# Performance work log

Measured on AMD Instinct MI355X. Metric: run time of the kernel, lower is better.

The kernel has to match this reference:

```python
import jax, jax.numpy as jnp
import numpy as np

EPS = 1e-5

# The 8 fixed sobel kernels from the original module. Summing convolutions with
# the same input equals one convolution with the summed kernel, so we embed the
# four 3x3 kernels (pad=1) into 5x5 (pad=2) and precombine everything into a
# single depthwise 5x5 kernel (exactly the math of detect_edge_1/2 summed).
_K3 = [
    [[2, 4, 2], [0, 0, 0], [-2, -4, -2]],
    [[4, 2, 0], [2, 0, -2], [0, -2, -4]],
    [[2, 0, -2], [4, 0, -4], [2, 0, -2]],
    [[0, -2, -4], [2, 0, -2], [4, 2, 0]],
]
_K5 = [
    [[0, 0, 0, 0, 0], [0, -2, -4, -2, 0], [-1, -4, 0, 4, 1], [0, 2, 4, 2, 0], [0, 0, 0, 0, 0]],
    [[0, 0, -1, 0, 0], [0, -2, -4, 2, 0], [0, -4, 0, 4, 0], [0, -2, 4, 2, 0], [0, 0, 1, 0, 0]],
    [[0, 0, 1, 0, 0], [0, -2, 4, 2, 0], [0, -4, 0, 4, 0], [0, -2, -4, 2, 0], [0, 0, -1, 0, 0]],
    [[0, 0, 0, 0, 0], [0, 2, 4, 2, 0], [-1, -4, 0, 4, 1], [0, -2, -4, -2, 0], [0, 0, 0, 0, 0]],
]

def _combined_sobel_kernel():
    k = np.zeros((5, 5), dtype=np.float32)
    for k3 in _K3:
        k[1:4, 1:4] += np.asarray(k3, dtype=np.float32)
    for k5 in _K5:
        k += np.asarray(k5, dtype=np.float32)
    return jnp.asarray(k)

SOBEL_K = _combined_sobel_kernel()  # [5,5]


def _conv2d(x, w, b, pad):
    # x: [N,C,H,W], w: [O,I,kh,kw]
    y = jax.lax.conv_general_dilated(
        x, w, window_strides=(1, 1), padding=[(pad, pad), (pad, pad)],
        dimension_numbers=('NCHW', 'OIHW', 'NCHW'))
    return y + b[None, :, None, None]


def _bn_relu(y, gamma, beta):
    # BatchNorm2d in training mode: per-channel batch stats over (N,H,W),
    # biased variance, eps=1e-5.
    m = jnp.mean(y, axis=(0, 2, 3), keepdims=True)
    v = jnp.mean(jnp.square(y - m), axis=(0, 2, 3), keepdims=True)
    yn = (y - m) * jax.lax.rsqrt(v + EPS)
    return jax.nn.relu(yn * gamma[None, :, None, None] + beta[None, :, None, None])


def _single_conv(x, w, b, gamma, beta, pad):
    return _bn_relu(_conv2d(x, w, b, pad), gamma, beta)


def _sobel(x):
    # Fused depthwise conv replacing the per-channel loops over 8 kernels.
    C = x.shape[1]
    w = jnp.broadcast_to(SOBEL_K[None, None], (C, 1, 5, 5))
    return jax.lax.conv_general_dilated(
        x, w, window_strides=(1, 1), padding=[(2, 2), (2, 2)],
        dimension_numbers=('NCHW', 'OIHW', 'NCHW'), feature_group_count=C)


def setup_inputs() -> dict:
    key = jax.random.key(0)
    ks = jax.random.split(key, 16)
    Cin, Cout = 64, 128
    Ch = Cout // 2
    B, H, W = 8, 160, 160
    s = 0.05
    d = {
        'input_f': jax.random.normal(ks[0], (B, Cin, H, W), jnp.float32),
        'w1': jax.random.normal(ks[1], (Cout, Cin, 1, 1), jnp.float32) * s,
        'b1': jnp.zeros((Cout,), jnp.float32),
        'g1': jnp.ones((Cout,), jnp.float32),
        'be1': jnp.zeros((Cout,), jnp.float32),
        'w2': jax.random.normal(ks[2], (Ch, Cout, 3, 3), jnp.float32) * s,
        'b2': jnp.zeros((Ch,), jnp.float32),
        'g2': jnp.ones((Ch,), jnp.float32),
        'be2': jnp.zeros((Ch,), jnp.float32),
        'w3': jax.random.normal(ks[3], (Ch, Ch, 3, 3), jnp.float32) * s,
        'b3': jnp.zeros((Ch,), jnp.float32),
        'g3': jnp.ones((Ch,), jnp.float32),
        'be3': jnp.zeros((Ch,), jnp.float32),
        'w4': jax.random.normal(ks[4], (Ch, Cin, 3, 3), jnp.float32) * s,
        'b4': jnp.zeros((Ch,), jnp.float32),
        'g4': jnp.ones((Ch,), jnp.float32),
        'be4': jnp.zeros((Ch,), jnp.float32),
    }
    return d


def reference(input_f, w1, b1, g1, be1, w2, b2, g2, be2, w3, b3, g3, be3, w4, b4, g4, be4):
    c1 = _single_conv(input_f, w1, b1, g1, be1, pad=0)   # [B,Cout,H,W]
    c2 = _single_conv(c1, w2, b2, g2, be2, pad=1)        # [B,Cout//2,H,W]
    edge = _sobel(c2)                                    # depthwise sobel sum
    c3 = _single_conv(edge, w3, b3, g3, be3, pad=1)
    skip = _single_conv(input_f, w4, b4, g4, be4, pad=1)
    return jnp.concatenate([skip, c3], axis=1)           # [B,Cout,H,W]
```

## Files before the change

### kernel.cpp

```cpp
#include <hip/hip_runtime.h>

typedef unsigned short u16;
typedef unsigned int u32;
typedef __attribute__((ext_vector_type(8))) short bf16x8;
typedef __attribute__((ext_vector_type(4))) float f32x4;

#define WD 160
#define HW 25600
#define NPIXF 204800.0f
#define BNEPS 1e-5f
#define SLOTB 6553600ll
#define BATB  13107200ll

__device__ __forceinline__ float bf2f(u16 u){ return __uint_as_float(((u32)u)<<16); }
__device__ __forceinline__ u16 f2bf(float f){ u32 x=__float_as_uint(f); return (u16)((x + 0x7FFFu + ((x>>16)&1u))>>16); }
__device__ __forceinline__ u32 pack2(float a,float b){ return (u32)f2bf(a) | ((u32)f2bf(b)<<16); }

__device__ __forceinline__ f32x4 MF(bf16x8 a, bf16x8 b, f32x4 c){
  return __builtin_amdgcn_mfma_f32_16x16x32_bf16(a, b, c, 0, 0, 0);
}
__device__ __forceinline__ void gload16(const void* g, void* l){
  __builtin_amdgcn_global_load_lds((const __attribute__((address_space(1))) void*)(g),
                                   (__attribute__((address_space(3))) void*)(l), 16, 0, 0);
}

__global__ __launch_bounds__(256) void k_prepw(
    const float* __restrict__ w1, const float* __restrict__ w2,
    const float* __restrict__ w3, const float* __restrict__ w4,
    u16* __restrict__ wp1, u16* __restrict__ wp2,
    u16* __restrict__ wp3, u16* __restrict__ wp4)
{
  int t = blockIdx.x*256 + threadIdx.x;
  if (t < 8192){
    int i = t&7, oc = (t>>3)&127, kc = (t>>10)&3, icb = t>>12;
    wp1[t] = f2bf(w1[oc*64 + icb*32 + kc*8 + i]);
  }
  int u = t - 8192;
  if (u >= 0 && u < 73728){
    int i = u&7, oc = (u>>3)&63, kc = (u>>9)&3, v = u>>11;
    int icb = (v*57)>>9; int tap = v - icb*9;
    wp2[u] = f2bf(w2[(oc*128 + icb*32 + kc*8 + i)*9 + tap]);
  }
  int u3 = t - (8192+73728);
  if (u3 >= 0 && u3 < 36864){
    int k = u3&31, oc = (u3>>5)&63, v = u3>>11;
    int icb = (v >= 9) ? 1 : 0; int tap = v - icb*9;
    int phys = u3 ^ (((oc>>1)&3)<<3);
    wp3[phys] = f2bf(w3[(oc*64 + icb*32 + k)*9 + tap]);
    wp4[phys] = f2bf(w4[(oc*64 + icb*32 + k)*9 + tap]);
  }
}

__global__ __launch_bounds__(256,2) void k_conv1(
    const float* __restrict__ x, const u16* __restrict__ wp1,
    char* __restrict__ dout, float* __restrict__ stats, int nslot)
{
  __shared__ __align__(16) char Xs[16384];
  __shared__ __align__(16) char Ws[8192];
  const int tid = threadIdx.x, lane = tid&63, w = tid>>6;
  const int l15 = lane&15, kc = lane>>4;
  const int b = blockIdx.y, px0 = blockIdx.x*256;
  const float* xb = x + (size_t)b*64*HW;

  f32x4 acc[4][8];
  for (int t=0;t<4;++t) for (int o=0;o<8;++o) acc[t][o] = (f32x4){0.f,0.f,0.f,0.f};

  int a1off[4];
  for (int t=0;t<4;++t){
    int px = (w*4+t)*16 + l15;
    a1off[t] = px*64 + ((kc ^ ((px>>1)&3))<<4);
  }
  const int wboff = kc*2048 + l15*16;

  for (int icb=0; icb<2; ++icb){
    __syncthreads();
    for (int it=0; it<16; ++it){
      int s = it*256 + tid;
      int icp = s >> 8, px = s & 255;
      const float* p = xb + (size_t)(icb*32 + icp*2)*HW + px0 + px;
      float v0 = p[0], v1 = p[HW];
      int phys = px*64 + (((icp>>2) ^ ((px>>1)&3))<<4) + (icp&3)*4;
      *(u32*)(Xs + phys) = pack2(v0, v1);
    }
    for (int it=0; it<2; ++it){
      int s = it*256 + tid;
      gload16(wp1 + (size_t)icb*4096 + s*8, Ws + (it*256 + (tid & ~63))*16);
    }
    asm volatile("s_waitcnt vmcnt(0)" ::: "memory");
    __syncthreads();
    bf16x8 a[4], bv[8];
#pragma unroll
    for (int t=0;t<4;++t) a[t] = *(const bf16x8*)(Xs + a1off[t]);
#pragma unroll
    for (int o=0;o<8;++o) bv[o] = *(const bf16x8*)(Ws + o*256 + wboff);
#pragma unroll
    for (int t=0;t<4;++t)
#pragma unroll
      for (int o=0;o<8;++o)
        acc[t][o] = MF(a[t], bv[o], acc[t][o]);
  }

  u16* c1 = (u16*)(dout + (size_t)b*BATB);
  float sa[8], sq[8];
  for (int o=0;o<8;++o){ sa[o]=0.f; sq[o]=0.f; }
  for (int t=0;t<4;++t){
    int pxb = px0 + (w*4+t)*16 + kc*4;
    for (int o=0;o<8;++o){
      int oc = o*16 + l15;
#pragma unroll
      for (int r=0;r<4;++r){
        float v = acc[t][o][r];
        c1[(size_t)(pxb + r)*128 + oc] = f2bf(v);
        sa[o]+=v; sq[o]+=v*v;
      }
    }
  }
  const int slot = (blockIdx.y*gridDim.x + blockIdx.x) & (nslot-1);
  for (int o=0;o<8;++o){
    float s1_=sa[o], s2_=sq[o];
    s1_+=__shfl_xor(s1_,16); s2_+=__shfl_xor(s2_,16);
    s1_+=__shfl_xor(s1_,32); s2_+=__shfl_xor(s2_,32);
    if (lane < 16){
      float* p = stats + ((size_t)slot*128 + o*16 + l15)*4;
      atomicAdd(p, s1_); atomicAdd(p+1, s2_);
    }
  }
}

__global__ void k_fold(const float* __restrict__ src, float* __restrict__ dst, int nslot){
  int c = threadIdx.x; if (c >= 128) return;
  float sm=0.f, sq=0.f;
  for (int s=0;s<nslot;++s){ const float* p = src + ((size_t)s*128 + c)*4; sm+=p[0]; sq+=p[1]; }
  dst[c*2] = sm; dst[c*2+1] = sq;
}

__global__ __launch_bounds__(256) void k_bn1(
    char* __restrict__ dout, const float* __restrict__ f1,
    const float* __restrict__ g1, const float* __restrict__ be1)
{
  __shared__ float asc[128], abi[128];
  int tid = threadIdx.x;
  if (tid < 128){
    float m = f1[tid*2]/NPIXF;
    float v = f1[tid*2+1]/NPIXF - m*m;
    float sc = g1[tid]*rsqrtf(v + BNEPS);
    asc[tid] = sc; abi[tid] = be1[tid] - m*sc;
  }
  __syncthreads();
  int b = blockIdx.y;
  size_t r = ((size_t)blockIdx.x*256 + tid)*8;
  int c0 = (int)(r & 127);
  const u16* src = (const u16*)(dout + (size_t)b*BATB) + r;
  u16* dst = (u16*)(dout + (size_t)b*BATB + SLOTB) + r;
  uint4 q = *(const uint4*)src;
  u32 wv[4] = {q.x,q.y,q.z,q.w};
#pragma unroll
  for (int j=0;j<4;++j){
    float lo = bf2f((u16)(wv[j]&0xFFFFu)), hi = bf2f((u16)(wv[j]>>16));
    lo = fmaxf(0.f, lo*asc[c0+2*j]   + abi[c0+2*j]);
    hi = fmaxf(0.f, hi*asc[c0+2*j+1] + abi[c0+2*j+1]);
    wv[j] = pack2(lo, hi);
  }
  *(uint4*)dst = make_uint4(wv[0],wv[1],wv[2],wv[3]);
}

__global__ __launch_bounds__(256,2) void k_conv2(
    char* __restrict__ dout, const u16* __restrict__ wp2,
    float* __restrict__ statsO, const u16* __restrict__ zeros, int nslot)
{
  __shared__ __align__(16) char Xs[24576];
  __shared__ __align__(16) char Ws[36864];
  const int tid = threadIdx.x, lane = tid&63, w = tid>>6;
  const int l15 = lane&15, kc = lane>>4;
  const int b = blockIdx.z, gx0 = blockIdx.x*32, gy0 = blockIdx.y*8;
  const u16* c1a = (const u16*)(dout + (size_t)b*BATB + SLOTB);
  u16* raw2 = (u16*)(dout + (size_t)b*BATB);

  f32x4 acc[4][4];
  for (int t=0;t<4;++t) for (int o=0;o<4;++o) acc[t][o] = (f32x4){0.f,0.f,0.f,0.f};

  int xon[2][3];
  for (int h=0;h<2;++h) for (int dx=0;dx<3;++dx){
    int xi = l15 + h*16 + dx;
    xon[h][dx] = xi*64 + ((kc ^ ((xi>>1)&3))<<4);
  }
  const int wboff = kc*1024 + l15*16;

  for (int icb=0; icb<4; ++icb){
    __syncthreads();
    for (int it=0; it<6; ++it){
      int s = it*256 + tid;
      int p = s>>2, sub = s&3;
      int yy = (int)(((u32)p*241u)>>13);
      int xi = p - yy*34;
      int gy = gy0 - 1 + yy, gx = gx0 - 1 + xi;
      int c = sub ^ ((xi>>1)&3);
      const u16* src = zeros;
      if (p < 340 && (unsigned)gy < 160u && (unsigned)gx < 160u)
        src = c1a + ((size_t)(gy*WD+gx)*128 + icb*32 + c*8);
      gload16(src, Xs + (it*256 + (tid & ~63))*16);
    }
    for (int it=0; it<9; ++it){
      int s = it*256 + tid;
      gload16(wp2 + (size_t)icb*18432 + s*8, Ws + (it*256 + (tid & ~63))*16);
    }
    asm volatile("s_waitcnt vmcnt(0)" ::: "memory");
    __syncthreads();
#pragma unroll
    for (int tap=0; tap<9; ++tap){
      const int dy = tap/3, dx = tap - dy*3;
      bf16x8 a[4], bv[4];
#pragma unroll
      for (int t=0;t<4;++t)
        a[t] = *(const bf16x8*)(Xs + (2*w + (t>>1) + dy)*2176 + xon[t&1][dx]);
#pragma unroll
      for (int o=0;o<4;++o)
        bv[o] = *(const bf16x8*)(Ws + tap*4096 + o*256 + wboff);
#pragma unroll
      for (int t=0;t<4;++t)
#pragma unroll
        for (int o=0;o<4;++o)
          acc[t][o] = MF(a[t], bv[o], acc[t][o]);
    }
  }

  float sa[4]={0,0,0,0}, sq[4]={0,0,0,0};
  for (int t=0;t<4;++t){
    int gy = gy0 + 2*w + (t>>1);
    int gxb = gx0 + (t&1)*16 + kc*4;
    for (int o=0;o<4;++o){
      int oc = o*16 + l15;
#pragma unroll
      for (int r=0;r<4;++r){
        float v = acc[t][o][r];
        raw2[(size_t)(gy*WD + gxb + r)*64 + oc] = f2bf(v);
        sa[o]+=v; sq[o]+=v*v;
      }
    }
  }
  int slot = (blockIdx.x + 5*(blockIdx.y + 20*blockIdx.z)) & (nslot-1);
  for (int o=0;o<4;++o){
    float s1_=sa[o], s2_=sq[o];
    s1_+=__shfl_xor(s1_,16); s2_+=__shfl_xor(s2_,16);
    s1_+=__shfl_xor(s1_,32); s2_+=__shfl_xor(s2_,32);
    if (lane<16){
      float* p = statsO + ((size_t)slot*128 + o*16 + l15)*4;
      atomicAdd(p,s1_); atomicAdd(p+1,s2_);
    }
  }
}

__global__ __launch_bounds__(256) void k_sobel(
    char* __restrict__ dout, const float* __restrict__ f2,
    const float* __restrict__ g2, const float* __restrict__ be2)
{
  __shared__ float asc[64], abi[64];
  int tid = threadIdx.x;
  if (tid < 64){
    float m = f2[tid*2]/NPIXF, v = f2[tid*2+1]/NPIXF - m*m;
    float sc = g2[tid]*rsqrtf(v+BNEPS);
    asc[tid]=sc; abi[tid]=be2[tid]-m*sc;
  }
  __syncthreads();
  int b = blockIdx.z, cb = blockIdx.y;
  int px = blockIdx.x*256 + tid;
  int y = (int)(((u32)px*52429u)>>23);
  int x = px - y*WD;
  const u16* raw2 = (const u16*)(dout + (size_t)b*BATB);
  u16* edge = (u16*)(dout + (size_t)b*BATB + 3276800);
  float av[8] = {0,0,0,0,0,0,0,0};
  auto TAP = [&](int dy, int dx, float wt){
    int yy = y+dy, xx = x+dx;
    if ((unsigned)yy>=160u || (unsigned)xx>=160u) return;
    uint4 q = *(const uint4*)(raw2 + ((size_t)(yy*WD+xx)*64 + cb*8));
    u32 ww[4] = {q.x,q.y,q.z,q.w};
#pragma unroll
    for (int j=0;j<4;++j){
      float lo = bf2f((u16)(ww[j]&0xFFFFu)), hi = bf2f((u16)(ww[j]>>16));
      lo = fmaxf(0.f, lo*asc[cb*8+2*j]   + abi[cb*8+2*j]);
      hi = fmaxf(0.f, hi*asc[cb*8+2*j+1] + abi[cb*8+2*j+1]);
      av[2*j]   += wt*lo;
      av[2*j+1] += wt*hi;
    }
  };
  TAP(-1,-1,4.f); TAP(-1,0,4.f);
  TAP(0,-2,-2.f); TAP(0,-1,-8.f); TAP(0,1,8.f); TAP(0,2,2.f);
  TAP(1,0,-4.f);  TAP(1,1,-4.f);
  uint4 o;
  o.x = pack2(av[0],av[1]); o.y = pack2(av[2],av[3]);
  o.z = pack2(av[4],av[5]); o.w = pack2(av[6],av[7]);
  *(uint4*)(edge + ((size_t)px*64 + cb*8)) = o;
}

template<bool XIN>
__global__ __launch_bounds__(256,2) void k_conv34(
    char* __restrict__ dout, const float* __restrict__ x,
    const u16* __restrict__ wp, float* __restrict__ statsO,
    const u16* __restrict__ zeros, int nslot)
{
  __shared__ __align__(16) char Xs[24576];
  __shared__ __align__(16) char Ws[36864];
  const int tid = threadIdx.x, lane = tid&63, w = tid>>6;
  const int l15 = lane&15, kc = lane>>4;
  const int b = blockIdx.z, gx0 = blockIdx.x*32, gy0 = blockIdx.y*8;
  const float* xb = XIN ? (x + (size_t)b*64*HW) : nullptr;
  const u16* edge = XIN ? nullptr : (const u16*)(dout + (size_t)b*BATB + 3276800);
  float* out = XIN ? (float*)(dout + (size_t)b*BATB)
                   : (float*)(dout + (size_t)b*BATB + SLOTB);

  f32x4 acc[4][4];
  for (int m=0;m<4;++m) for (int t=0;t<4;++t) acc[m][t] = (f32x4){0.f,0.f,0.f,0.f};

  int xon[2][3];
  for (int h=0;h<2;++h) for (int dx=0;dx<3;++dx){
    int xi = l15 + h*16 + dx;
    xon[h][dx] = xi*64 + ((kc ^ ((xi>>1)&3))<<4);
  }
  int wko[4];
  for (int m=0;m<4;++m){
    int oc = m*16 + l15;
    wko[m] = oc*64 + ((kc ^ ((oc>>1)&3))<<4);
  }

  for (int icb=0; icb<2; ++icb){
    __syncthreads();
    if (XIN){
      for (int it=0; it<22; ++it){
        int s = it*256 + tid; if (s >= 5440) break;
        int yq = (int)(((u32)(s>>5)*965u)>>14);
        int rem = s - yq*544;
        int icp = (int)(((u32)rem*241u)>>13);
        int xi = rem - icp*34;
        int gy = gy0-1+yq, gx = gx0-1+xi;
        float v0=0.f, v1=0.f;
        if ((unsigned)gy<160u && (unsigned)gx<160u){
          const float* p = xb + (size_t)(icb*32 + icp*2)*HW + gy*WD + gx;
          v0 = p[0]; v1 = p[HW];
        }
        int phys = (yq*34 + xi)*64 + (((icp>>2) ^ ((xi>>1)&3))<<4) + (icp&3)*4;
        *(u32*)(Xs + phys) = pack2(v0, v1);
      }
    } else {
      for (int it=0; it<6; ++it){
        int s = it*256 + tid;
        int p = s>>2, sub = s&3;
        int yy = (int)(((u32)p*241u)>>13);
        int xi = p - yy*34;
        int gy = gy0-1+yy, gx = gx0-1+xi;
        int c = sub ^ ((xi>>1)&3);
        const u16* src = zeros;
        if (p<340 && (unsigned)gy<160u && (unsigned)gx<160u)
          src = edge + ((size_t)(gy*WD+gx)*64 + icb*32 + c*8);
        gload16(src, Xs + (it*256 + (tid & ~63))*16);
      }
    }
    for (int it=0; it<9; ++it){
      int s = it*256 + tid;
      gload16(wp + (size_t)icb*18432 + s*8, Ws + (it*256 + (tid & ~63))*16);
    }
    asm volatile("s_waitcnt vmcnt(0)" ::: "memory");
    __syncthreads();
#pragma unroll
    for (int tap=0; tap<9; ++tap){
      const int dy = tap/3, dx = tap - dy*3;
      bf16x8 a[4], bv[4];
#pragma unroll
      for (int m=0;m<4;++m) a[m] = *(const bf16x8*)(Ws + tap*4096 + wko[m]);
#pragma unroll
      for (int t=0;t<4;++t) bv[t] = *(const bf16x8*)(Xs + (2*w + (t>>1) + dy)*2176 + xon[t&1][dx]);
#pragma unroll
      for (int m=0;m<4;++m)
#pragma unroll
        for (int t=0;t<4;++t)
          acc[m][t] = MF(a[m], bv[t], acc[m][t]);
    }
  }

  float sa[4][4], sq[4][4];
  for (int m=0;m<4;++m) for (int r=0;r<4;++r){ sa[m][r]=0.f; sq[m][r]=0.f; }
  for (int m=0;m<4;++m){
    for (int t=0;t<4;++t){
      int gy = gy0 + 2*w + (t>>1);
      int gx = gx0 + (t&1)*16 + l15;
#pragma unroll
      for (int r=0;r<4;++r){
        float v = acc[m][t][r];
        out[(size_t)(m*16 + kc*4 + r)*HW + gy*WD + gx] = v;
        sa[m][r]+=v; sq[m][r]+=v*v;
      }
    }
  }
  int slot = (blockIdx.x + 5*(blockIdx.y + 20*blockIdx.z)) & (nslot-1);
  for (int m=0;m<4;++m)
    for (int r=0;r<4;++r){
      float s1_=sa[m][r], s2_=sq[m][r];
      s1_+=__shfl_xor(s1_,1); s2_+=__shfl_xor(s2_,1);
      s1_+=__shfl_xor(s1_,2); s2_+=__shfl_xor(s2_,2);
      s1_+=__shfl_xor(s1_,4); s2_+=__shfl_xor(s2_,4);
      s1_+=__shfl_xor(s1_,8); s2_+=__shfl_xor(s2_,8);
      if (l15==0){
        float* p = statsO + ((size_t)slot*128 + m*16 + kc*4 + r)*4;
        atomicAdd(p,s1_); atomicAdd(p+1,s2_);
      }
    }
}

__global__ __launch_bounds__(256) void k_bnrelu(
    float* __restrict__ io, const float* __restrict__ f3, const float* __restrict__ f4,
    const float* __restrict__ g3, const float* __restrict__ be3,
    const float* __restrict__ g4, const float* __restrict__ be4)
{
  size_t e = ((size_t)blockIdx.x*256 + threadIdx.x)*8;
  int cg = (int)((e/HW) & 127);
  float* p = io + (size_t)blockIdx.y*3276800 + e;
  float sm,sq,gg,bb;
  if (cg>=64){ int c=cg-64; sm=f3[c*2]; sq=f3[c*2+1]; gg=g3[c]; bb=be3[c]; }
  else       {             sm=f4[cg*2]; sq=f4[cg*2+1]; gg=g4[cg]; bb=be4[cg]; }
  float m = sm/NPIXF;
  float v = sq/NPIXF - m*m;
  float sc = gg*rsqrtf(v + BNEPS);
  float bi = bb - m*sc;
  float4 a = *(float4*)p;
  float4 bq = *(float4*)(p+4);
  a.x=fmaxf(0.f,a.x*sc+bi); a.y=fmaxf(0.f,a.y*sc+bi);
  a.z=fmaxf(0.f,a.z*sc+bi); a.w=fmaxf(0.f,a.w*sc+bi);
  bq.x=fmaxf(0.f,bq.x*sc+bi); bq.y=fmaxf(0.f,bq.y*sc+bi);
  bq.z=fmaxf(0.f,bq.z*sc+bi); bq.w=fmaxf(0.f,bq.w*sc+bi);
  *(float4*)p = a;
  *(float4*)(p+4) = bq;
}

extern "C" void kernel_launch(void* const* d_in, const int* in_sizes, int n_in,
                              void* d_out, int out_size, void* d_ws, size_t ws_size,
                              hipStream_t stream)
{
  const float* x   = (const float*)d_in[0];
  const float* w1  = (const float*)d_in[1];
  const float* g1  = (const float*)d_in[3];
  const float* be1 = (const float*)d_in[4];
  const float* w2  = (const float*)d_in[5];
  const float* g2  = (const float*)d_in[7];
  const float* be2 = (const float*)d_in[8];
  const float* w3  = (const float*)d_in[9];
  const float* g3  = (const float*)d_in[11];
  const float* be3 = (const float*)d_in[12];
  const float* w4  = (const float*)d_in[13];
  const float* g4  = (const float*)d_in[15];
  const float* be4 = (const float*)d_in[16];
  (void)in_sizes; (void)n_in; (void)out_size;

  int nslot = 32;
  auto need = [&](int ns)->size_t{
    return (size_t)4*ns*128*4*4 + 4096 + (size_t)(8192+73728+36864+36864)*2 + 256;
  };
  while (nslot > 1 && need(nslot) > ws_size) nslot >>= 1;
  if (need(nslot) > ws_size) return;

  char* ws = (char*)d_ws;
  float* S = (float*)ws;
  size_t stg = (size_t)nslot*128*4;
  float* S0=S, *S1=S+stg, *S2=S+2*stg, *S3=S+3*stg;
  float* F = S + 4*stg;
  u16* wp1 = (u16*)(F + 1024);
  u16* wp2 = wp1 + 8192;
  u16* wp3 = wp2 + 73728;
  u16* wp4 = wp3 + 36864;
  u16* zeros = wp4 + 36864;

  hipMemsetAsync(S, 0, 4*stg*sizeof(float), stream);
  hipMemsetAsync(zeros, 0, 256, stream);

  k_prepw<<<464, 256, 0, stream>>>(w1, w2, w3, w4, wp1, wp2, wp3, wp4);
  k_conv1<<<dim3(100,8), 256, 0, stream>>>(x, wp1, (char*)d_out, S0, nslot);
  k_fold<<<1, 128, 0, stream>>>(S0, F, nslot);
  k_bn1<<<dim3(1600,8), 256, 0, stream>>>((char*)d_out, F, g1, be1);
  k_conv2<<<dim3(5,20,8), 256, 0, stream>>>((char*)d_out, wp2, S1, zeros, nslot);
  k_fold<<<1, 128, 0, stream>>>(S1, F+256, nslot);
  k_sobel<<<dim3(100,8,8), 256, 0, stream>>>((char*)d_out, F+256, g2, be2);
  k_conv34<false><<<dim3(5,20,8), 256, 0, stream>>>((char*)d_out, nullptr, wp3, S2, zeros, nslot);
  k_conv34<true ><<<dim3(5,20,8), 256, 0, stream>>>((char*)d_out, x, wp4, S3, zeros, nslot);
  k_fold<<<1, 128, 0, stream>>>(S2, F+512, nslot);
  k_fold<<<1, 128, 0, stream>>>(S3, F+768, nslot);
  k_bnrelu<<<dim3(1600,8), 256, 0, stream>>>((float*)d_out, F+512, F+768, g3, be3, g4, be4);
}
```

Baseline: 399.0 us.

## Read conv weights directly from global, merge conv3/conv4 launches, halve conv1 tile

Conv weights are no longer staged through LDS. Each wave loads its MFMA weight fragments straight from global memory, so conv1, conv2 and conv34 lose the weight LDS buffers and the matching swizzle in prepw. conv1 now tiles 128 pixels per block across a 2x2 wave split and loads both input-channel halves before a single barrier. conv3 and conv4 run as one launch with a job index taken from blockIdx.z, and each block loads all of its input channels into a 48KB LDS buffer up front. The zero-fill source now uses a per-lane offset into a larger zero buffer. The aims are fewer barriers, lower LDS pressure and fewer launches, at the cost of repeated global or L2 weight reads and a larger LDS footprint in conv34.

```diff
diff --git a/kernel.cpp b/kernel.cpp
--- a/kernel.cpp
+++ b/kernel.cpp
@@ -45,9 +45,8 @@
   if (u3 >= 0 && u3 < 36864){
     int k = u3&31, oc = (u3>>5)&63, v = u3>>11;
     int icb = (v >= 9) ? 1 : 0; int tap = v - icb*9;
-    int phys = u3 ^ (((oc>>1)&3)<<3);
-    wp3[phys] = f2bf(w3[(oc*64 + icb*32 + k)*9 + tap]);
-    wp4[phys] = f2bf(w4[(oc*64 + icb*32 + k)*9 + tap]);
+    wp3[u3] = f2bf(w3[(oc*64 + icb*32 + k)*9 + tap]);
+    wp4[u3] = f2bf(w4[(oc*64 + icb*32 + k)*9 + tap]);
   }
 }
 
@@ -55,58 +54,53 @@
     const float* __restrict__ x, const u16* __restrict__ wp1,
     char* __restrict__ dout, float* __restrict__ stats, int nslot)
 {
-  __shared__ __align__(16) char Xs[16384];
-  __shared__ __align__(16) char Ws[8192];
+  __shared__ __align__(16) char Xs[2][8192];
   const int tid = threadIdx.x, lane = tid&63, w = tid>>6;
   const int l15 = lane&15, kc = lane>>4;
-  const int b = blockIdx.y, px0 = blockIdx.x*256;
+  const int b = blockIdx.y, px0 = blockIdx.x*128;
   const float* xb = x + (size_t)b*64*HW;
 
-  f32x4 acc[4][8];
-  for (int t=0;t<4;++t) for (int o=0;o<8;++o) acc[t][o] = (f32x4){0.f,0.f,0.f,0.f};
-
+#pragma unroll 4
+  for (int it=0; it<16; ++it){
+    int s = it*256 + tid;
+    int icb = s >> 11, sl = s & 2047;
+    int icp = sl >> 7, px = sl & 127;
+    const float* p = xb + (size_t)(icb*32 + icp*2)*HW + px0 + px;
+    float v0 = p[0], v1 = p[HW];
+    int phys = px*64 + (((icp>>2) ^ ((px>>1)&3))<<4) + (icp&3)*4;
+    *(u32*)(Xs[icb] + phys) = pack2(v0, v1);
+  }
+  __syncthreads();
+
+  f32x4 acc[4][4];
+  for (int t=0;t<4;++t) for (int o=0;o<4;++o) acc[t][o] = (f32x4){0.f,0.f,0.f,0.f};
+  const int och = (w>>1)*64;
   int a1off[4];
   for (int t=0;t<4;++t){
-    int px = (w*4+t)*16 + l15;
+    int px = (w&1)*64 + t*16 + l15;
     a1off[t] = px*64 + ((kc ^ ((px>>1)&3))<<4);
   }
-  const int wboff = kc*2048 + l15*16;
-
+#pragma unroll
   for (int icb=0; icb<2; ++icb){
-    __syncthreads();
-    for (int it=0; it<16; ++it){
-      int s = it*256 + tid;
-      int icp = s >> 8, px = s & 255;
-      const float* p = xb + (size_t)(icb*32 + icp*2)*HW + px0 + px;
-      float v0 = p[0], v1 = p[HW];
-      int phys = px*64 + (((icp>>2) ^ ((px>>1)&3))<<4) + (icp&3)*4;
-      *(u32*)(Xs + phys) = pack2(v0, v1);
-    }
-    for (int it=0; it<2; ++it){
-      int s = it*256 + tid;
-      gload16(wp1 + (size_t)icb*4096 + s*8, Ws + (it*256 + (tid & ~63))*16);
-    }
-    asm volatile("s_waitcnt vmcnt(0)" ::: "memory");
-    __syncthreads();
-    bf16x8 a[4], bv[8];
-#pragma unroll
-    for (int t=0;t<4;++t) a[t] = *(const bf16x8*)(Xs + a1off[t]);
-#pragma unroll
-    for (int o=0;o<8;++o) bv[o] = *(const bf16x8*)(Ws + o*256 + wboff);
+    bf16x8 a[4], bw[4];
+#pragma unroll
+    for (int t=0;t<4;++t) a[t] = *(const bf16x8*)(Xs[icb] + a1off[t]);
+#pragma unroll
+    for (int o=0;o<4;++o)
+      bw[o] = *(const bf16x8*)(wp1 + ((size_t)(icb*4 + kc)*128 + och + o*16 + l15)*8);
 #pragma unroll
     for (int t=0;t<4;++t)
 #pragma unroll
-      for (int o=0;o<8;++o)
-        acc[t][o] = MF(a[t], bv[o], acc[t][o]);
+      for (int o=0;o<4;++o)
+        acc[t][o] = MF(a[t], bw[o], acc[t][o]);
   }
 
   u16* c1 = (u16*)(dout + (size_t)b*BATB);
-  float sa[8], sq[8];
-  for (int o=0;o<8;++o){ sa[o]=0.f; sq[o]=0.f; }
+  float sa[4]={0,0,0,0}, sq[4]={0,0,0,0};
   for (int t=0;t<4;++t){
-    int pxb = px0 + (w*4+t)*16 + kc*4;
-    for (int o=0;o<8;++o){
-      int oc = o*16 + l15;
+    int pxb = px0 + (w&1)*64 + t*16 + kc*4;
+    for (int o=0;o<4;++o){
+      int oc = och + o*16 + l15;
 #pragma unroll
       for (int r=0;r<4;++r){
         float v = acc[t][o][r];
@@ -116,12 +110,12 @@
     }
   }
   const int slot = (blockIdx.y*gridDim.x + blockIdx.x) & (nslot-1);
-  for (int o=0;o<8;++o){
+  for (int o=0;o<4;++o){
     float s1_=sa[o], s2_=sq[o];
     s1_+=__shfl_xor(s1_,16); s2_+=__shfl_xor(s2_,16);
     s1_+=__shfl_xor(s1_,32); s2_+=__shfl_xor(s2_,32);
     if (lane < 16){
-      float* p = stats + ((size_t)slot*128 + o*16 + l15)*4;
+      float* p = stats + ((size_t)slot*128 + och + o*16 + l15)*4;
       atomicAdd(p, s1_); atomicAdd(p+1, s2_);
     }
   }
@@ -169,7 +163,6 @@
     float* __restrict__ statsO, const u16* __restrict__ zeros, int nslot)
 {
   __shared__ __align__(16) char Xs[24576];
-  __shared__ __align__(16) char Ws[36864];
   const int tid = threadIdx.x, lane = tid&63, w = tid>>6;
   const int l15 = lane&15, kc = lane>>4;
   const int b = blockIdx.z, gx0 = blockIdx.x*32, gy0 = blockIdx.y*8;
@@ -184,7 +177,6 @@
     int xi = l15 + h*16 + dx;
     xon[h][dx] = xi*64 + ((kc ^ ((xi>>1)&3))<<4);
   }
-  const int wboff = kc*1024 + l15*16;
 
   for (int icb=0; icb<4; ++icb){
     __syncthreads();
@@ -195,32 +187,28 @@
       int xi = p - yy*34;
       int gy = gy0 - 1 + yy, gx = gx0 - 1 + xi;
       int c = sub ^ ((xi>>1)&3);
-      const u16* src = zeros;
+      const u16* src = zeros + ((tid&63)<<3);
       if (p < 340 && (unsigned)gy < 160u && (unsigned)gx < 160u)
         src = c1a + ((size_t)(gy*WD+gx)*128 + icb*32 + c*8);
       gload16(src, Xs + (it*256 + (tid & ~63))*16);
     }
-    for (int it=0; it<9; ++it){
-      int s = it*256 + tid;
-      gload16(wp2 + (size_t)icb*18432 + s*8, Ws + (it*256 + (tid & ~63))*16);
-    }
     asm volatile("s_waitcnt vmcnt(0)" ::: "memory");
     __syncthreads();
 #pragma unroll
     for (int tap=0; tap<9; ++tap){
       const int dy = tap/3, dx = tap - dy*3;
-      bf16x8 a[4], bv[4];
+      bf16x8 a[4], bw[4];
+#pragma unroll
+      for (int o=0;o<4;++o)
+        bw[o] = *(const bf16x8*)(wp2 + ((size_t)((icb*9 + tap)*4 + kc)*64 + o*16 + l15)*8);
 #pragma unroll
       for (int t=0;t<4;++t)
         a[t] = *(const bf16x8*)(Xs + (2*w + (t>>1) + dy)*2176 + xon[t&1][dx]);
 #pragma unroll
-      for (int o=0;o<4;++o)
-        bv[o] = *(const bf16x8*)(Ws + tap*4096 + o*256 + wboff);
-#pragma unroll
       for (int t=0;t<4;++t)
 #pragma unroll
         for (int o=0;o<4;++o)
-          acc[t][o] = MF(a[t], bv[o], acc[t][o]);
+          acc[t][o] = MF(a[t], bw[o], acc[t][o]);
     }
   }
 
@@ -292,82 +280,83 @@
   *(uint4*)(edge + ((size_t)px*64 + cb*8)) = o;
 }
 
-template<bool XIN>
 __global__ __launch_bounds__(256,2) void k_conv34(
     char* __restrict__ dout, const float* __restrict__ x,
-    const u16* __restrict__ wp, float* __restrict__ statsO,
+    const u16* __restrict__ wp3, const u16* __restrict__ wp4,
+    float* __restrict__ st3, float* __restrict__ st4,
     const u16* __restrict__ zeros, int nslot)
 {
-  __shared__ __align__(16) char Xs[24576];
-  __shared__ __align__(16) char Ws[36864];
+  __shared__ __align__(16) char Xs[49152];
   const int tid = threadIdx.x, lane = tid&63, w = tid>>6;
   const int l15 = lane&15, kc = lane>>4;
-  const int b = blockIdx.z, gx0 = blockIdx.x*32, gy0 = blockIdx.y*8;
-  const float* xb = XIN ? (x + (size_t)b*64*HW) : nullptr;
-  const u16* edge = XIN ? nullptr : (const u16*)(dout + (size_t)b*BATB + 3276800);
-  float* out = XIN ? (float*)(dout + (size_t)b*BATB)
+  const int bz = blockIdx.z, b = bz>>1, job = bz&1;
+  const int gx0 = blockIdx.x*32, gy0 = blockIdx.y*8;
+  const u16* wp = job ? wp4 : wp3;
+  float* statsO = job ? st4 : st3;
+  float* out = job ? (float*)(dout + (size_t)b*BATB)
                    : (float*)(dout + (size_t)b*BATB + SLOTB);
+
+  if (job){
+    const float* xb = x + (size_t)b*64*HW;
+#pragma unroll 4
+    for (int it=0; it<43; ++it){
+      int s = it*256 + tid; if (s >= 10880) break;
+      int icb = (s >= 5440) ? 1 : 0;
+      int sl = s - icb*5440;
+      int yq = (int)(((u32)(sl>>5)*965u)>>14);
+      int rem = sl - yq*544;
+      int icp = (int)(((u32)rem*241u)>>13);
+      int xi = rem - icp*34;
+      int gy = gy0-1+yq, gx = gx0-1+xi;
+      float v0=0.f, v1=0.f;
+      if ((unsigned)gy<160u && (unsigned)gx<160u){
+        const float* p = xb + (size_t)(icb*32 + icp*2)*HW + gy*WD + gx;
+        v0 = p[0]; v1 = p[HW];
+      }
+      int phys = icb*24576 + (yq*34 + xi)*64 + (((icp>>2) ^ ((xi>>1)&3))<<4) + (icp&3)*4;
+      *(u32*)(Xs + phys) = pack2(v0, v1);
+    }
+  } else {
+    const u16* edge = (const u16*)(dout + (size_t)b*BATB + 3276800);
+    for (int it=0; it<12; ++it){
+      int s = it*256 + tid;
+      int icb = s >> 11;
+      icb = (s >= 1536) ? 1 : 0;
+      int sl = s - icb*1536;
+      int p = sl>>2, sub = sl&3;
+      int yy = (int)(((u32)p*241u)>>13);
+      int xi = p - yy*34;
+      int gy = gy0-1+yy, gx = gx0-1+xi;
+      int c = sub ^ ((xi>>1)&3);
+      const u16* src = zeros + ((tid&63)<<3);
+      if (p<340 && (unsigned)gy<160u && (unsigned)gx<160u)
+        src = edge + ((size_t)(gy*WD+gx)*64 + icb*32 + c*8);
+      gload16(src, Xs + (it*256 + (tid & ~63))*16);
+    }
+    asm volatile("s_waitcnt vmcnt(0)" ::: "memory");
+  }
+  __syncthreads();
 
   f32x4 acc[4][4];
   for (int m=0;m<4;++m) for (int t=0;t<4;++t) acc[m][t] = (f32x4){0.f,0.f,0.f,0.f};
-
   int xon[2][3];
   for (int h=0;h<2;++h) for (int dx=0;dx<3;++dx){
     int xi = l15 + h*16 + dx;
     xon[h][dx] = xi*64 + ((kc ^ ((xi>>1)&3))<<4);
   }
-  int wko[4];
-  for (int m=0;m<4;++m){
-    int oc = m*16 + l15;
-    wko[m] = oc*64 + ((kc ^ ((oc>>1)&3))<<4);
-  }
-
+
+#pragma unroll
   for (int icb=0; icb<2; ++icb){
-    __syncthreads();
-    if (XIN){
-      for (int it=0; it<22; ++it){
-        int s = it*256 + tid; if (s >= 5440) break;
-        int yq = (int)(((u32)(s>>5)*965u)>>14);
-        int rem = s - yq*544;
-        int icp = (int)(((u32)rem*241u)>>13);
-        int xi = rem - icp*34;
-        int gy = gy0-1+yq, gx = gx0-1+xi;
-        float v0=0.f, v1=0.f;
-        if ((unsigned)gy<160u && (unsigned)gx<160u){
-          const float* p = xb + (size_t)(icb*32 + icp*2)*HW + gy*WD + gx;
-          v0 = p[0]; v1 = p[HW];
-        }
-        int phys = (yq*34 + xi)*64 + (((icp>>2) ^ ((xi>>1)&3))<<4) + (icp&3)*4;
-        *(u32*)(Xs + phys) = pack2(v0, v1);
-      }
-    } else {
-      for (int it=0; it<6; ++it){
-        int s = it*256 + tid;
-        int p = s>>2, sub = s&3;
-        int yy = (int)(((u32)p*241u)>>13);
-        int xi = p - yy*34;
-        int gy = gy0-1+yy, gx = gx0-1+xi;
-        int c = sub ^ ((xi>>1)&3);
-        const u16* src = zeros;
-        if (p<340 && (unsigned)gy<160u && (unsigned)gx<160u)
-          src = edge + ((size_t)(gy*WD+gx)*64 + icb*32 + c*8);
-        gload16(src, Xs + (it*256 + (tid & ~63))*16);
-      }
-    }
-    for (int it=0; it<9; ++it){
-      int s = it*256 + tid;
-      gload16(wp + (size_t)icb*18432 + s*8, Ws + (it*256 + (tid & ~63))*16);
-    }
-    asm volatile("s_waitcnt vmcnt(0)" ::: "memory");
-    __syncthreads();
 #pragma unroll
     for (int tap=0; tap<9; ++tap){
       const int dy = tap/3, dx = tap - dy*3;
       bf16x8 a[4], bv[4];
 #pragma unroll
-      for (int m=0;m<4;++m) a[m] = *(const bf16x8*)(Ws + tap*4096 + wko[m]);
-#pragma unroll
-      for (int t=0;t<4;++t) bv[t] = *(const bf16x8*)(Xs + (2*w + (t>>1) + dy)*2176 + xon[t&1][dx]);
+      for (int m=0;m<4;++m)
+        a[m] = *(const bf16x8*)(wp + ((size_t)((icb*9+tap)*64 + m*16 + l15)*32 + kc*8));
+#pragma unroll
+      for (int t=0;t<4;++t)
+        bv[t] = *(const bf16x8*)(Xs + icb*24576 + (2*w + (t>>1) + dy)*2176 + xon[t&1][dx]);
 #pragma unroll
       for (int m=0;m<4;++m)
 #pragma unroll
@@ -451,7 +440,7 @@
 
   int nslot = 32;
   auto need = [&](int ns)->size_t{
-    return (size_t)4*ns*128*4*4 + 4096 + (size_t)(8192+73728+36864+36864)*2 + 256;
+    return (size_t)4*ns*128*4*4 + 4096 + (size_t)(8192+73728+36864+36864)*2 + 1024;
   };
   while (nslot > 1 && need(nslot) > ws_size) nslot >>= 1;
   if (need(nslot) > ws_size) return;
@@ -468,17 +457,16 @@
   u16* zeros = wp4 + 36864;
 
   hipMemsetAsync(S, 0, 4*stg*sizeof(float), stream);
-  hipMemsetAsync(zeros, 0, 256, stream);
+  hipMemsetAsync(zeros, 0, 1024, stream);
 
   k_prepw<<<464, 256, 0, stream>>>(w1, w2, w3, w4, wp1, wp2, wp3, wp4);
-  k_conv1<<<dim3(100,8), 256, 0, stream>>>(x, wp1, (char*)d_out, S0, nslot);
+  k_conv1<<<dim3(200,8), 256, 0, stream>>>(x, wp1, (char*)d_out, S0, nslot);
   k_fold<<<1, 128, 0, stream>>>(S0, F, nslot);
   k_bn1<<<dim3(1600,8), 256, 0, stream>>>((char*)d_out, F, g1, be1);
   k_conv2<<<dim3(5,20,8), 256, 0, stream>>>((char*)d_out, wp2, S1, zeros, nslot);
   k_fold<<<1, 128, 0, stream>>>(S1, F+256, nslot);
   k_sobel<<<dim3(100,8,8), 256, 0, stream>>>((char*)d_out, F+256, g2, be2);
-  k_conv34<false><<<dim3(5,20,8), 256, 0, stream>>>((char*)d_out, nullptr, wp3, S2, zeros, nslot);
-  k_conv34<true ><<<dim3(5,20,8), 256, 0, stream>>>((char*)d_out, x, wp4, S3, zeros, nslot);
+  k_conv34<<<dim3(5,20,16), 256, 0, stream>>>((char*)d_out, x, wp3, wp4, S2, S3, zeros, nslot);
   k_fold<<<1, 128, 0, stream>>>(S2, F+512, nslot);
   k_fold<<<1, 128, 0, stream>>>(S3, F+768, nslot);
   k_bnrelu<<<dim3(1600,8), 256, 0, stream>>>((float*)d_out, F+512, F+768, g3, be3, g4, be4);
```

Result: no change. 392.4 us (-1.7%).
